# Performance work log

Measured on AMD Instinct MI355X. Metric: run time of the kernel, lower is better.

Reference implementation:

```python
import jax, jax.numpy as jnp
import numpy as np

TEMP = 0.05
MOMENTUM = 0.2
SMOOTH = 0.1
TAU_W = 0.09
NUM_SAMPLES = 100000
NUM_FEATURES = 256
BATCH = 256


def _l2norm(x, axis=1, eps=1e-12):
    return x / jnp.maximum(jnp.linalg.norm(x, axis=axis, keepdims=True), eps)


def setup_inputs() -> dict:
    key = jax.random.key(0)
    k1, k2, k3, k4 = jax.random.split(key, 4)
    inputs1 = jax.random.normal(k1, (BATCH, NUM_FEATURES), dtype=jnp.float32)
    inputs2 = jax.random.normal(k2, (BATCH, NUM_FEATURES), dtype=jnp.float32)
    features = jax.random.normal(k3, (NUM_SAMPLES, NUM_FEATURES), dtype=jnp.float32)
    features = _l2norm(features)  # memory bank holds unit-norm centroids
    targets = jax.random.randint(k4, (BATCH,), 0, NUM_SAMPLES)
    return {"inputs1": inputs1, "inputs2": inputs2, "features": features, "targets": targets}


def reference(inputs1, inputs2, features, targets):
    # ---- ClusterMemory.forward (mode='wgm') ----
    x1 = _l2norm(inputs1)                      # F.normalize(inputs1)
    x2 = _l2norm(inputs2)                      # F.normalize(inputs2)
    outputs = (x1 @ features.T) / TEMP         # [B, N] logits vs memory bank
    regression = (x2 @ features.T) / TEMP      # [B, N]

    logp = jax.nn.log_softmax(outputs, axis=1)
    # CrossEntropyLoss
    loss_c = -jnp.mean(jnp.take_along_axis(logp, targets[:, None], axis=1))
    # SoftEntropySmooth: smoothed mix of soft targets (detached) and one-hot
    onehot = jax.nn.one_hot(targets, features.shape[0], dtype=logp.dtype)
    smooth_t = jax.lax.stop_gradient(
        (1.0 - SMOOTH) * jax.nn.softmax(regression, axis=1) + SMOOTH * onehot
    )
    loss_s = jnp.sum(jnp.mean(-smooth_t * logp, axis=0))

    # ---- CM_WgtMean memory update: per-cluster segment softmax + scatter ----
    N = features.shape[0]
    d = jnp.sum(x1 * features[targets], axis=1)            # [B] sim to own centroid
    logits = -d / TAU_W
    segmax = jax.ops.segment_max(logits, targets, num_segments=N)   # [N]
    e = jnp.exp(logits - segmax[targets])                  # stable per-segment exp
    denom = jax.ops.segment_sum(e, targets, num_segments=N)
    w = e / denom[targets]                                 # segment softmax weights
    wmean = jax.ops.segment_sum(w[:, None] * x1, targets, num_segments=N)  # [N, D]
    counts = jax.ops.segment_sum(jnp.ones_like(d), targets, num_segments=N)
    upd = _l2norm(MOMENTUM * features + (1.0 - MOMENTUM) * wmean)
    new_features = jnp.where((counts > 0)[:, None], upd, features)

    return loss_c, loss_s, new_features
```

## Files before the change

### kernel.cpp

```cpp
#include <hip/hip_runtime.h>
#include <stdint.h>
#include <stddef.h>

#define TEMP      0.05f
#define INV_TEMP  20.0f
#define MOMENTUM  0.2f
#define SMOOTH    0.1f
#define TAU_W     0.09f
#define NSAMP     100000
#define NFEAT     256
#define BATCH     256
#define SHIFT     20.0f
#define MT        64

typedef float  f32x4  __attribute__((ext_vector_type(4)));
typedef float  f32x2  __attribute__((ext_vector_type(2)));
typedef short  short8 __attribute__((ext_vector_type(8)));
typedef unsigned int u32x2 __attribute__((ext_vector_type(2)));

__device__ __forceinline__ short f2bf(float f) {
    uint32_t u = __builtin_bit_cast(uint32_t, f);
    u = (u + 0x7fffu + ((u >> 16) & 1u)) >> 16;
    return (short)u;
}

__device__ __forceinline__ void mfma_bf16(f32x4& c, short8 a, short8 b) {
    asm("v_mfma_f32_16x16x32_bf16 %0, %1, %2, %0" : "+v"(c) : "v"(a), "v"(b));
}

__device__ __forceinline__ float block_reduce_sum256(float v, float* scratch) {
    for (int o = 32; o > 0; o >>= 1) v += __shfl_down(v, o, 64);
    int lane = threadIdx.x & 63, wid = threadIdx.x >> 6;
    if (lane == 0) scratch[wid] = v;
    __syncthreads();
    if (threadIdx.x == 0)
        scratch[4] = scratch[0] + scratch[1] + scratch[2] + scratch[3];
    __syncthreads();
    return scratch[4];
}

__global__ void k_prep(const float* __restrict__ in1, const float* __restrict__ in2,
                       const float* __restrict__ F, const int* __restrict__ tgt,
                       float* __restrict__ x1n, short* __restrict__ Xb,
                       float* __restrict__ dvec,
                       float* __restrict__ Z1, float* __restrict__ Z2, float* __restrict__ S12) {
    __shared__ float scratch[8];
    int b = blockIdx.x;
    int k = threadIdx.x;
    float v1 = in1[b * NFEAT + k];
    float v2 = in2[b * NFEAT + k];
    float n1 = block_reduce_sum256(v1 * v1, scratch);
    float n2 = block_reduce_sum256(v2 * v2, scratch);
    float x1 = v1 / fmaxf(sqrtf(n1), 1e-12f);
    float x2 = v2 / fmaxf(sqrtf(n2), 1e-12f);
    x1n[b * NFEAT + k] = x1;
    int g = b >> 5, r = b & 31;
    Xb[(g * 64 + r) * NFEAT + k]      = f2bf(x1);
    Xb[(g * 64 + 32 + r) * NFEAT + k] = f2bf(x2);
    int t = tgt[b];
    float dv = block_reduce_sum256(x1 * F[(size_t)t * NFEAT + k], scratch);
    if (k == 0) {
        dvec[b] = dv;
        Z1[b] = 0.f; Z2[b] = 0.f; S12[b] = 0.f;
    }
}

__global__ void __launch_bounds__(512)
k_main(const float* __restrict__ F, const short* __restrict__ Xb,
       float* __restrict__ out,
       float* __restrict__ Z1, float* __restrict__ Z2, float* __restrict__ S12) {
    __shared__ short lfs[MT * NFEAT];
    int tid = threadIdx.x;
    int m0 = blockIdx.x * MT;

    #pragma unroll
    for (int rr = 0; rr < 8; ++rr) {
        int c   = rr * 512 + tid;
        int row = c >> 6, cc = c & 63;
        int grow = m0 + row;
        f32x4 v = {0.f, 0.f, 0.f, 0.f};
        if (grow < NSAMP)
            v = *(const f32x4*)(F + (size_t)grow * NFEAT + cc * 4);
        uint32_t p0 = (uint32_t)(uint16_t)f2bf(v[0]) | ((uint32_t)(uint16_t)f2bf(v[1]) << 16);
        uint32_t p1 = (uint32_t)(uint16_t)f2bf(v[2]) | ((uint32_t)(uint16_t)f2bf(v[3]) << 16);
        int off = row * 512 + ((cc * 8) ^ ((row & 7) << 4));
        *(u32x2*)((char*)lfs + off) = (u32x2){p0, p1};
        if (grow < NSAMP) {
            float* op = out + 2 + (size_t)grow * NFEAT + cc * 4;
            *(f32x2*)op       = (f32x2){v[0], v[1]};
            *(f32x2*)(op + 2) = (f32x2){v[2], v[3]};
        }
    }
    __syncthreads();

    int w = tid >> 6, lane = tid & 63;
    int l15 = lane & 15, lg = lane >> 4;

    f32x4 acc[4][4] = {};
    const short* xbase = Xb + (size_t)(w * 64) * NFEAT;

    #pragma unroll
    for (int kk = 0; kk < 8; ++kk) {
        int kb = kk * 64 + lg * 16;
        short8 a[4], bf[4];
        #pragma unroll
        for (int cf = 0; cf < 4; ++cf)
            bf[cf] = *(const short8*)(xbase + (cf * 16 + l15) * NFEAT + kk * 32 + lg * 8);
        #pragma unroll
        for (int mf = 0; mf < 4; ++mf) {
            int row = mf * 16 + l15;
            a[mf] = *(const short8*)((const char*)lfs + row * 512 + (kb ^ ((row & 7) << 4)));
        }
        #pragma unroll
        for (int mf = 0; mf < 4; ++mf)
            #pragma unroll
            for (int cf = 0; cf < 4; ++cf)
                mfma_bf16(acc[mf][cf], a[mf], bf[cf]);
    }

    #pragma unroll
    for (int cf = 0; cf < 2; ++cf) {
        float z1 = 0.f, z2 = 0.f, s12 = 0.f;
        #pragma unroll
        for (int mf = 0; mf < 4; ++mf) {
            #pragma unroll
            for (int q = 0; q < 4; ++q) {
                int grow = m0 + mf * 16 + lg * 4 + q;
                if (grow < NSAMP) {
                    float l1 = acc[mf][cf][q] * INV_TEMP;
                    float e1 = __expf(l1 - SHIFT);
                    float e2 = __expf(acc[mf][cf + 2][q] * INV_TEMP - SHIFT);
                    z1 += e1; z2 += e2; s12 += e2 * l1;
                }
            }
        }
        z1  += __shfl_xor(z1, 16);  z1  += __shfl_xor(z1, 32);
        z2  += __shfl_xor(z2, 16);  z2  += __shfl_xor(z2, 32);
        s12 += __shfl_xor(s12, 16); s12 += __shfl_xor(s12, 32);
        if (lane < 16) {
            int b = w * 32 + cf * 16 + lane;
            atomicAdd(&Z1[b], z1);
            atomicAdd(&Z2[b], z2);
            atomicAdd(&S12[b], s12);
        }
    }
}

__global__ void k_update(const float* __restrict__ F, const int* __restrict__ tgt,
                         const float* __restrict__ dvec, const float* __restrict__ x1n,
                         float* __restrict__ out) {
    __shared__ float scratch[8];
    int b = blockIdx.x, k = threadIdx.x;
    int t = tgt[b];
    for (int bp = 0; bp < b; ++bp)
        if (tgt[bp] == t) return;
    float m = -1e30f;
    for (int bp = 0; bp < BATCH; ++bp)
        if (tgt[bp] == t) m = fmaxf(m, -dvec[bp] / TAU_W);
    float denom = 0.f;
    for (int bp = 0; bp < BATCH; ++bp)
        if (tgt[bp] == t) denom += expf(-dvec[bp] / TAU_W - m);
    float wmean = 0.f;
    for (int bp = 0; bp < BATCH; ++bp)
        if (tgt[bp] == t) {
            float wq = expf(-dvec[bp] / TAU_W - m) / denom;
            wmean += wq * x1n[bp * NFEAT + k];
        }
    float upd = MOMENTUM * F[(size_t)t * NFEAT + k] + (1.f - MOMENTUM) * wmean;
    float nrm = block_reduce_sum256(upd * upd, scratch);
    out[2 + (size_t)t * NFEAT + k] = upd / fmaxf(sqrtf(nrm), 1e-12f);
}

__global__ void k_loss(const float* __restrict__ dvec, const float* __restrict__ Z1,
                       const float* __restrict__ Z2, const float* __restrict__ S12,
                       float* __restrict__ out) {
    __shared__ float scratch[8];
    int b = threadIdx.x;
    float L1   = SHIFT + logf(Z1[b]);
    float lpt  = dvec[b] * INV_TEMP - L1;
    float ce12 = S12[b] / Z2[b];
    float lc = -lpt;
    float ls = (1.f - SMOOTH) * (L1 - ce12) + SMOOTH * (-lpt);
    float sc = block_reduce_sum256(lc, scratch);
    float ss = block_reduce_sum256(ls, scratch);
    if (b == 0) {
        out[0] = sc / (float)BATCH;
        out[1] = ss / (float)BATCH;
    }
}

extern "C" void kernel_launch(void* const* d_in, const int* in_sizes, int n_in,
                              void* d_out, int out_size, void* d_ws, size_t ws_size,
                              hipStream_t stream) {
    const float* in1 = (const float*)d_in[0];
    const float* in2 = (const float*)d_in[1];
    const float* F   = (const float*)d_in[2];
    const int*   tgt = (const int*)d_in[3];
    float* out = (float*)d_out;

    char* ws = (char*)d_ws;
    float* x1n = (float*)ws;
    short* Xb  = (short*)(ws + 262144);
    float* dv  = (float*)(ws + 524288);
    float* Z1  = (float*)(ws + 525312);
    float* Z2  = (float*)(ws + 526336);
    float* S12 = (float*)(ws + 527360);

    hipLaunchKernelGGL(k_prep, dim3(BATCH), dim3(256), 0, stream,
                       in1, in2, F, tgt, x1n, Xb, dv, Z1, Z2, S12);
    hipLaunchKernelGGL(k_main, dim3((NSAMP + MT - 1) / MT), dim3(512), 0, stream,
                       F, Xb, out, Z1, Z2, S12);
    hipLaunchKernelGGL(k_update, dim3(BATCH), dim3(256), 0, stream,
                       F, tgt, dv, x1n, out);
    hipLaunchKernelGGL(k_loss, dim3(1), dim3(256), 0, stream,
                       dv, Z1, Z2, S12, out);
}
```

Baseline: 289.9 us.

## Split feature-bank copy into separate streaming kernel and batch loads in main GEMM

Moves the full memory-bank copy into its own grid-stride kernel using nontemporal stores, so the GEMM kernel no longer writes the output bank. The GEMM kernel now issues all eight row loads before converting them to bf16, to increase memory-level parallelism. The update kernel caches targets and precomputed logits in shared memory and divides by the softmax denominator once. The cost is a second full read of the feature bank.

```diff
diff --git a/kernel.cpp b/kernel.cpp
--- a/kernel.cpp
+++ b/kernel.cpp
@@ -37,6 +37,18 @@
         scratch[4] = scratch[0] + scratch[1] + scratch[2] + scratch[3];
     __syncthreads();
     return scratch[4];
+}
+
+__global__ void __launch_bounds__(256)
+k_copy(const float* __restrict__ F, float* __restrict__ out) {
+    const size_t total = (size_t)NSAMP * NFEAT / 4;
+    size_t stride = (size_t)gridDim.x * 256;
+    for (size_t i = (size_t)blockIdx.x * 256 + threadIdx.x; i < total; i += stride) {
+        f32x4 v = *(const f32x4*)(F + i * 4);
+        float* op = out + 2 + i * 4;
+        __builtin_nontemporal_store(f32x2{v[0], v[1]}, (f32x2*)op);
+        __builtin_nontemporal_store(f32x2{v[2], v[3]}, (f32x2*)(op + 2));
+    }
 }
 
 __global__ void k_prep(const float* __restrict__ in1, const float* __restrict__ in2,
@@ -67,29 +79,29 @@
 
 __global__ void __launch_bounds__(512)
 k_main(const float* __restrict__ F, const short* __restrict__ Xb,
-       float* __restrict__ out,
        float* __restrict__ Z1, float* __restrict__ Z2, float* __restrict__ S12) {
     __shared__ short lfs[MT * NFEAT];
     int tid = threadIdx.x;
     int m0 = blockIdx.x * MT;
 
+    f32x4 v[8];
     #pragma unroll
     for (int rr = 0; rr < 8; ++rr) {
         int c   = rr * 512 + tid;
         int row = c >> 6, cc = c & 63;
         int grow = m0 + row;
-        f32x4 v = {0.f, 0.f, 0.f, 0.f};
+        v[rr] = f32x4{0.f, 0.f, 0.f, 0.f};
         if (grow < NSAMP)
-            v = *(const f32x4*)(F + (size_t)grow * NFEAT + cc * 4);
-        uint32_t p0 = (uint32_t)(uint16_t)f2bf(v[0]) | ((uint32_t)(uint16_t)f2bf(v[1]) << 16);
-        uint32_t p1 = (uint32_t)(uint16_t)f2bf(v[2]) | ((uint32_t)(uint16_t)f2bf(v[3]) << 16);
+            v[rr] = *(const f32x4*)(F + (size_t)grow * NFEAT + cc * 4);
+    }
+    #pragma unroll
+    for (int rr = 0; rr < 8; ++rr) {
+        int c   = rr * 512 + tid;
+        int row = c >> 6, cc = c & 63;
+        uint32_t p0 = (uint32_t)(uint16_t)f2bf(v[rr][0]) | ((uint32_t)(uint16_t)f2bf(v[rr][1]) << 16);
+        uint32_t p1 = (uint32_t)(uint16_t)f2bf(v[rr][2]) | ((uint32_t)(uint16_t)f2bf(v[rr][3]) << 16);
         int off = row * 512 + ((cc * 8) ^ ((row & 7) << 4));
         *(u32x2*)((char*)lfs + off) = (u32x2){p0, p1};
-        if (grow < NSAMP) {
-            float* op = out + 2 + (size_t)grow * NFEAT + cc * 4;
-            *(f32x2*)op       = (f32x2){v[0], v[1]};
-            *(f32x2*)(op + 2) = (f32x2){v[2], v[3]};
-        }
     }
     __syncthreads();
 
@@ -149,23 +161,27 @@
 __global__ void k_update(const float* __restrict__ F, const int* __restrict__ tgt,
                          const float* __restrict__ dvec, const float* __restrict__ x1n,
                          float* __restrict__ out) {
+    __shared__ int   stgt[BATCH];
+    __shared__ float slog[BATCH];
     __shared__ float scratch[8];
     int b = blockIdx.x, k = threadIdx.x;
-    int t = tgt[b];
+    stgt[k] = tgt[k];
+    slog[k] = -dvec[k] * (1.0f / TAU_W);
+    __syncthreads();
+    int t = stgt[b];
     for (int bp = 0; bp < b; ++bp)
-        if (tgt[bp] == t) return;
+        if (stgt[bp] == t) return;
     float m = -1e30f;
     for (int bp = 0; bp < BATCH; ++bp)
-        if (tgt[bp] == t) m = fmaxf(m, -dvec[bp] / TAU_W);
+        if (stgt[bp] == t) m = fmaxf(m, slog[bp]);
     float denom = 0.f;
     for (int bp = 0; bp < BATCH; ++bp)
-        if (tgt[bp] == t) denom += expf(-dvec[bp] / TAU_W - m);
+        if (stgt[bp] == t) denom += expf(slog[bp] - m);
     float wmean = 0.f;
     for (int bp = 0; bp < BATCH; ++bp)
-        if (tgt[bp] == t) {
-            float wq = expf(-dvec[bp] / TAU_W - m) / denom;
-            wmean += wq * x1n[bp * NFEAT + k];
-        }
+        if (stgt[bp] == t)
+            wmean += expf(slog[bp] - m) * x1n[bp * NFEAT + k];
+    wmean /= denom;
     float upd = MOMENTUM * F[(size_t)t * NFEAT + k] + (1.f - MOMENTUM) * wmean;
     float nrm = block_reduce_sum256(upd * upd, scratch);
     out[2 + (size_t)t * NFEAT + k] = upd / fmaxf(sqrtf(nrm), 1e-12f);
@@ -206,10 +222,11 @@
     float* Z2  = (float*)(ws + 526336);
     float* S12 = (float*)(ws + 527360);
 
+    hipLaunchKernelGGL(k_copy, dim3(2048), dim3(256), 0, stream, F, out);
     hipLaunchKernelGGL(k_prep, dim3(BATCH), dim3(256), 0, stream,
                        in1, in2, F, tgt, x1n, Xb, dv, Z1, Z2, S12);
     hipLaunchKernelGGL(k_main, dim3((NSAMP + MT - 1) / MT), dim3(512), 0, stream,
-                       F, Xb, out, Z1, Z2, S12);
+                       F, Xb, Z1, Z2, S12);
     hipLaunchKernelGGL(k_update, dim3(BATCH), dim3(256), 0, stream,
                        F, tgt, dv, x1n, out);
     hipLaunchKernelGGL(k_loss, dim3(1), dim3(256), 0, stream,
```

New measurement: 356.5 us. +23.0%, slower.
